# Performance work log

Measured on AMD Instinct MI355X. Metric: run time of the kernel, lower is better.

## Reference

```python
import jax, jax.numpy as jnp
import numpy as np

EPS = 1e-5


def _corr_matrix(A):
    # A: [n, f]. Standardize each column with unbiased std (torch.std default,
    # ddof=1), then all-pairs correlation as a single GEMM, matching
    # mean(x_std * y_std) over the batch dim for every column pair.
    n = A.shape[0]
    mu = A.mean(axis=0, keepdims=True)
    sd = A.std(axis=0, ddof=1, keepdims=True)
    As = (A - mu) / (sd + EPS)            # [n, f]
    return (As.T @ As) / n                 # [f, f]


def setup_inputs() -> dict:
    key = jax.random.key(0)
    kx, ky = jax.random.split(key)
    X = jax.random.normal(kx, (8192, 1024), dtype=jnp.float32)
    Y = jax.random.normal(ky, (8192, 1024), dtype=jnp.float32)
    return {"X": X, "Y": Y}


def reference(X, Y):
    f = X.shape[1]
    diff = _corr_matrix(X) - _corr_matrix(Y)          # [f, f]
    mask = jnp.triu(jnp.ones((f, f), dtype=diff.dtype), k=1)  # pairs i<j
    count = f * (f - 1) // 2
    loss = jnp.sum((diff * diff) * mask) / count
    return loss
```

## Files before the change

### kernel.cpp

```cpp
#include <hip/hip_runtime.h>
#include <hip/hip_bf16.h>
#include <stdint.h>

#define NROWS 8192
#define NF    1024
#define EPSV  1e-5f

typedef __attribute__((ext_vector_type(8))) short bf16x8;
typedef __attribute__((ext_vector_type(4))) float f32x4;

static __device__ __forceinline__ unsigned short f2bf(float v) {
    __hip_bfloat16 b = __float2bfloat16(v);
    return *reinterpret_cast<unsigned short*>(&b);
}

__global__ void stats_partial(const float* __restrict__ X, const float* __restrict__ Y,
                              float* __restrict__ psum, float* __restrict__ psq) {
    int cg    = blockIdx.x;
    int chunk = blockIdx.y;
    int mat   = blockIdx.z;
    const float* A = mat ? Y : X;
    int col = cg * 256 + threadIdx.x;
    const float* p = A + (size_t)(chunk * 128) * NF + col;
    float s = 0.f, sq = 0.f;
    #pragma unroll 4
    for (int i = 0; i < 128; ++i) {
        float v = p[(size_t)i * NF];
        s += v; sq += v * v;
    }
    int idx = (mat * 64 + chunk) * NF + col;
    psum[idx] = s;
    psq[idx]  = sq;
}

__global__ void stats_final(const float* __restrict__ psum, const float* __restrict__ psq,
                            float* __restrict__ mu, float* __restrict__ isd) {
    __shared__ float ls[4][64], lq[4][64];
    int mat  = blockIdx.y;
    int col0 = blockIdx.x * 64;
    int colq = threadIdx.x & 63;
    int g    = threadIdx.x >> 6;
    int col  = col0 + colq;
    float s = 0.f, sq = 0.f;
    #pragma unroll
    for (int k = 0; k < 16; ++k) {
        int idx = (mat * 64 + g * 16 + k) * NF + col;
        s  += psum[idx];
        sq += psq[idx];
    }
    ls[g][colq] = s; lq[g][colq] = sq;
    __syncthreads();
    if (g == 0) {
        s  = ls[0][colq] + ls[1][colq] + ls[2][colq] + ls[3][colq];
        sq = lq[0][colq] + lq[1][colq] + lq[2][colq] + lq[3][colq];
        float m   = s / (float)NROWS;
        float var = (sq - s * m) / (float)(NROWS - 1);
        var = fmaxf(var, 0.f);
        mu [mat * NF + col] = m;
        isd[mat * NF + col] = 1.0f / (sqrtf(var) + EPSV);
    }
}

__global__ void std_transpose(const float* __restrict__ X, const float* __restrict__ Y,
                              const float* __restrict__ mu, const float* __restrict__ isd,
                              unsigned short* __restrict__ Xst, unsigned short* __restrict__ Yst) {
    __shared__ unsigned short sbuf[64][68];
    __shared__ float smu[64], sisd[64];
    int ct  = blockIdx.x;
    int rt  = blockIdx.y;
    int mat = blockIdx.z;
    const float* A = mat ? Y : X;
    unsigned short* O = mat ? Yst : Xst;
    int tid = threadIdx.x;
    if (tid < 64) {
        smu[tid]  = mu [mat * NF + ct * 64 + tid];
        sisd[tid] = isd[mat * NF + ct * 64 + tid];
    }
    __syncthreads();
    #pragma unroll
    for (int it = 0; it < 4; ++it) {
        int idx = it * 256 + tid;
        int row = idx >> 4;
        int c4  = idx & 15;
        float4 v = *reinterpret_cast<const float4*>(
            A + (size_t)(rt * 64 + row) * NF + ct * 64 + c4 * 4);
        ushort4 o;
        o.x = f2bf((v.x - smu[c4 * 4 + 0]) * sisd[c4 * 4 + 0]);
        o.y = f2bf((v.y - smu[c4 * 4 + 1]) * sisd[c4 * 4 + 1]);
        o.z = f2bf((v.z - smu[c4 * 4 + 2]) * sisd[c4 * 4 + 2]);
        o.w = f2bf((v.w - smu[c4 * 4 + 3]) * sisd[c4 * 4 + 3]);
        *reinterpret_cast<ushort4*>(&sbuf[row][c4 * 4]) = o;
    }
    __syncthreads();
    {
        int c  = tid >> 2;
        int r8 = tid & 3;
        bf16x8 v0, v1;
        #pragma unroll
        for (int i = 0; i < 8; ++i) v0[i] = (short)sbuf[r8 * 16 + i][c];
        #pragma unroll
        for (int i = 0; i < 8; ++i) v1[i] = (short)sbuf[r8 * 16 + 8 + i][c];
        unsigned short* dst = O + (size_t)(ct * 64 + c) * NROWS + rt * 64 + r8 * 16;
        *reinterpret_cast<bf16x8*>(dst)     = v0;
        *reinterpret_cast<bf16x8*>(dst + 8) = v1;
    }
}

__global__ __launch_bounds__(256, 2) void gram_gemm(
    const unsigned short* __restrict__ Xst, const unsigned short* __restrict__ Yst,
    float* __restrict__ Cpart, int nsplit, int kper) {
    __shared__ short As[128 * 64];
    __shared__ short Bs[128 * 64];
    int tile = blockIdx.x, split = blockIdx.y, mat = blockIdx.z;
    int r = 0, t = tile;
    while (t >= 8 - r) { t -= 8 - r; ++r; }
    int c = r + t;
    const short* A = reinterpret_cast<const short*>(mat ? Yst : Xst);
    int tid = threadIdx.x, lane = tid & 63, wid = tid >> 6;
    int wr = wid >> 1, wc = wid & 1;
    f32x4 acc[4][4] = {};
    int k0 = split * kper;
    int nstep = kper >> 6;
    int r_loc = lane >> 3;
    int kc    = (lane & 7) ^ r_loc;

    for (int step = 0; step < nstep; ++step) {
        int kk = k0 + step * 64;
        __syncthreads();
        #pragma unroll
        for (int i = 0; i < 4; ++i) {
            int chunk = wid * 4 + i;
            int row = chunk * 8 + r_loc;
            const short* ga = A + (size_t)(r * 128 + row) * NROWS + kk + kc * 8;
            __builtin_amdgcn_global_load_lds(
                (const __attribute__((address_space(1))) void*)ga,
                (__attribute__((address_space(3))) void*)(As + chunk * 512), 16, 0, 0);
            const short* gb = A + (size_t)(c * 128 + row) * NROWS + kk + kc * 8;
            __builtin_amdgcn_global_load_lds(
                (const __attribute__((address_space(1))) void*)gb,
                (__attribute__((address_space(3))) void*)(Bs + chunk * 512), 16, 0, 0);
        }
        __syncthreads();
        bf16x8 af[4][2], bfr[4][2];
        #pragma unroll
        for (int fm = 0; fm < 4; ++fm) {
            int rowA = wr * 64 + fm * 16 + (lane & 15);
            int rowB = wc * 64 + fm * 16 + (lane & 15);
            #pragma unroll
            for (int h = 0; h < 2; ++h) {
                int kb = h * 4 + (lane >> 4);
                af [fm][h] = *reinterpret_cast<const bf16x8*>(
                    As + rowA * 64 + ((kb ^ (rowA & 7)) * 8));
                bfr[fm][h] = *reinterpret_cast<const bf16x8*>(
                    Bs + rowB * 64 + ((kb ^ (rowB & 7)) * 8));
            }
        }
        #pragma unroll
        for (int h = 0; h < 2; ++h)
            #pragma unroll
            for (int fm = 0; fm < 4; ++fm)
                #pragma unroll
                for (int fn = 0; fn < 4; ++fn)
                    acc[fm][fn] = __builtin_amdgcn_mfma_f32_16x16x32_bf16(
                        af[fm][h], bfr[fn][h], acc[fm][fn], 0, 0, 0);
    }

    float* Cp = Cpart + ((size_t)(mat * nsplit + split) * 36 + tile) * 16384;
    #pragma unroll
    for (int fm = 0; fm < 4; ++fm)
        #pragma unroll
        for (int fn = 0; fn < 4; ++fn)
            #pragma unroll
            for (int reg = 0; reg < 4; ++reg) {
                int row = wr * 64 + fm * 16 + (lane >> 4) * 4 + reg;
                int col = wc * 64 + fn * 16 + (lane & 15);
                Cp[row * 128 + col] = acc[fm][fn][reg];
            }
}

__global__ void reduce_loss(const float* __restrict__ Cpart, float* __restrict__ out,
                            int nsplit) {
    int tile = blockIdx.x, sub = blockIdx.y;
    int r = 0, t = tile;
    while (t >= 8 - r) { t -= 8 - r; ++r; }
    int c = r + t;
    const float inv_n = 1.0f / (float)NROWS;
    float s = 0.f;
    for (int e4 = threadIdx.x; e4 < 512; e4 += 256) {
        int row  = sub * 16 + (e4 >> 5);
        int col0 = (e4 & 31) * 4;
        float xs0 = 0.f, xs1 = 0.f, xs2 = 0.f, xs3 = 0.f;
        float ys0 = 0.f, ys1 = 0.f, ys2 = 0.f, ys3 = 0.f;
        for (int sp = 0; sp < nsplit; ++sp) {
            float4 vx = *reinterpret_cast<const float4*>(
                Cpart + ((size_t)sp * 36 + tile) * 16384 + row * 128 + col0);
            float4 vy = *reinterpret_cast<const float4*>(
                Cpart + ((size_t)(nsplit + sp) * 36 + tile) * 16384 + row * 128 + col0);
            xs0 += vx.x; xs1 += vx.y; xs2 += vx.z; xs3 += vx.w;
            ys0 += vy.x; ys1 += vy.y; ys2 += vy.z; ys3 += vy.w;
        }
        float dv[4] = {xs0 - ys0, xs1 - ys1, xs2 - ys2, xs3 - ys3};
        #pragma unroll
        for (int j = 0; j < 4; ++j) {
            int col = col0 + j;
            if (r == c && col <= row) continue;
            float d = dv[j] * inv_n;
            s += d * d;
        }
    }
    #pragma unroll
    for (int off = 32; off > 0; off >>= 1) s += __shfl_down(s, off, 64);
    __shared__ float wsum[4];
    int lane = threadIdx.x & 63, wid = threadIdx.x >> 6;
    if (lane == 0) wsum[wid] = s;
    __syncthreads();
    if (threadIdx.x == 0) {
        float tot = wsum[0] + wsum[1] + wsum[2] + wsum[3];
        atomicAdd(out, tot * (1.0f / 523776.0f));
    }
}

extern "C" void kernel_launch(void* const* d_in, const int* in_sizes, int n_in,
                              void* d_out, int out_size, void* d_ws, size_t ws_size,
                              hipStream_t stream) {
    const float* X = (const float*)d_in[0];
    const float* Y = (const float*)d_in[1];
    char* ws = (char*)d_ws;

    auto need = [](int ns) -> size_t {
        return ((size_t)32 << 20)
             + (size_t)2 * ns * 36 * 16384 * 4
             + ((size_t)512 << 10) * 2
             + ((size_t)8 << 10) * 2;
    };
    int nsplit = 8;
    if (ws_size < need(8)) nsplit = 4;
    if (ws_size < need(4)) nsplit = 2;
    if (ws_size < need(2)) nsplit = 1;
    int kper = NROWS / nsplit;

    unsigned short* Xst = (unsigned short*)(ws);
    unsigned short* Yst = (unsigned short*)(ws + ((size_t)16 << 20));
    float* Cpart = (float*)(ws + ((size_t)32 << 20));
    size_t cpart_sz = (size_t)2 * nsplit * 36 * 16384 * 4;
    float* psum = (float*)(ws + ((size_t)32 << 20) + cpart_sz);
    float* psq  = psum + 2 * 64 * NF;
    float* mu   = psq  + 2 * 64 * NF;
    float* isd  = mu   + 2 * NF;
    float* out  = (float*)d_out;

    hipMemsetAsync(out, 0, sizeof(float), stream);
    stats_partial<<<dim3(4, 64, 2), 256, 0, stream>>>(X, Y, psum, psq);
    stats_final<<<dim3(16, 2), 256, 0, stream>>>(psum, psq, mu, isd);
    std_transpose<<<dim3(16, 128, 2), 256, 0, stream>>>(X, Y, mu, isd, Xst, Yst);
    gram_gemm<<<dim3(36, nsplit, 2), 256, 0, stream>>>(Xst, Yst, Cpart, nsplit, kper);
    reduce_loss<<<dim3(36, 8), 256, 0, stream>>>(Cpart, out, nsplit);
}
```

Baseline: 179.2 us.

## Gram on raw bf16 data, apply standardization algebraically in fused double-buffered GEMM

Replaces the separate stats pass and standardize-transpose pass with one transpose kernel that converts raw inputs to bf16 and accumulates column sums from the bf16 values. The Gram GEMM now runs on unstandardized data and applies mean/std correction in its epilogue (C/n - mu_i mu_j) * isd_i * isd_j. X and Y are computed in the same workgroup with double-buffered LDS staging, and only their difference is written. This removes one full read pass over the inputs and halves partial-output traffic. In exchange, the centering is subtracted only after accumulation, so bf16 rounding of uncentered data can hurt accuracy when means are large. The split count also rises to 16 with an XCD-aware block swizzle.

```diff
diff --git a/kernel.cpp b/kernel.cpp
--- a/kernel.cpp
+++ b/kernel.cpp
@@ -13,24 +13,60 @@
     __hip_bfloat16 b = __float2bfloat16(v);
     return *reinterpret_cast<unsigned short*>(&b);
 }
-
-__global__ void stats_partial(const float* __restrict__ X, const float* __restrict__ Y,
-                              float* __restrict__ psum, float* __restrict__ psq) {
-    int cg    = blockIdx.x;
-    int chunk = blockIdx.y;
-    int mat   = blockIdx.z;
+static __device__ __forceinline__ float bf2f(unsigned short u) {
+    union { uint32_t i; float f; } cv; cv.i = (uint32_t)u << 16; return cv.f;
+}
+
+__global__ void transpose_stats(const float* __restrict__ X, const float* __restrict__ Y,
+                                unsigned short* __restrict__ Xst, unsigned short* __restrict__ Yst,
+                                float* __restrict__ psum, float* __restrict__ psq) {
+    __shared__ unsigned short sbuf[64][68];
+    int ct  = blockIdx.x;
+    int rt  = blockIdx.y;
+    int mat = blockIdx.z;
     const float* A = mat ? Y : X;
-    int col = cg * 256 + threadIdx.x;
-    const float* p = A + (size_t)(chunk * 128) * NF + col;
-    float s = 0.f, sq = 0.f;
-    #pragma unroll 4
-    for (int i = 0; i < 128; ++i) {
-        float v = p[(size_t)i * NF];
-        s += v; sq += v * v;
-    }
-    int idx = (mat * 64 + chunk) * NF + col;
-    psum[idx] = s;
-    psq[idx]  = sq;
+    unsigned short* O = mat ? Yst : Xst;
+    int tid = threadIdx.x;
+    #pragma unroll
+    for (int it = 0; it < 4; ++it) {
+        int idx = it * 256 + tid;
+        int row = idx >> 4;
+        int c4  = idx & 15;
+        float4 v = *reinterpret_cast<const float4*>(
+            A + (size_t)(rt * 64 + row) * NF + ct * 64 + c4 * 4);
+        ushort4 o;
+        o.x = f2bf(v.x); o.y = f2bf(v.y); o.z = f2bf(v.z); o.w = f2bf(v.w);
+        *reinterpret_cast<ushort4*>(&sbuf[row][c4 * 4]) = o;
+    }
+    __syncthreads();
+    {
+        int c  = tid >> 2;
+        int r8 = tid & 3;
+        bf16x8 v0, v1;
+        float s = 0.f, sq = 0.f;
+        #pragma unroll
+        for (int i = 0; i < 8; ++i) {
+            unsigned short u = sbuf[r8 * 16 + i][c];
+            v0[i] = (short)u;
+            float f = bf2f(u); s += f; sq += f * f;
+        }
+        #pragma unroll
+        for (int i = 0; i < 8; ++i) {
+            unsigned short u = sbuf[r8 * 16 + 8 + i][c];
+            v1[i] = (short)u;
+            float f = bf2f(u); s += f; sq += f * f;
+        }
+        unsigned short* dst = O + (size_t)(ct * 64 + c) * NROWS + rt * 64 + r8 * 16;
+        *reinterpret_cast<bf16x8*>(dst)     = v0;
+        *reinterpret_cast<bf16x8*>(dst + 8) = v1;
+        s  += __shfl_xor(s, 1);  s  += __shfl_xor(s, 2);
+        sq += __shfl_xor(sq, 1); sq += __shfl_xor(sq, 2);
+        if (r8 == 0) {
+            int pidx = (mat * 128 + rt) * NF + ct * 64 + c;
+            psum[pidx] = s;
+            psq[pidx]  = sq;
+        }
+    }
 }
 
 __global__ void stats_final(const float* __restrict__ psum, const float* __restrict__ psq,
@@ -43,8 +79,8 @@
     int col  = col0 + colq;
     float s = 0.f, sq = 0.f;
     #pragma unroll
-    for (int k = 0; k < 16; ++k) {
-        int idx = (mat * 64 + g * 16 + k) * NF + col;
+    for (int k = 0; k < 32; ++k) {
+        int idx = (mat * 128 + g * 32 + k) * NF + col;
         s  += psum[idx];
         sq += psq[idx];
     }
@@ -61,151 +97,131 @@
     }
 }
 
-__global__ void std_transpose(const float* __restrict__ X, const float* __restrict__ Y,
-                              const float* __restrict__ mu, const float* __restrict__ isd,
-                              unsigned short* __restrict__ Xst, unsigned short* __restrict__ Yst) {
-    __shared__ unsigned short sbuf[64][68];
-    __shared__ float smu[64], sisd[64];
-    int ct  = blockIdx.x;
-    int rt  = blockIdx.y;
-    int mat = blockIdx.z;
-    const float* A = mat ? Y : X;
-    unsigned short* O = mat ? Yst : Xst;
-    int tid = threadIdx.x;
-    if (tid < 64) {
-        smu[tid]  = mu [mat * NF + ct * 64 + tid];
-        sisd[tid] = isd[mat * NF + ct * 64 + tid];
-    }
-    __syncthreads();
-    #pragma unroll
-    for (int it = 0; it < 4; ++it) {
-        int idx = it * 256 + tid;
-        int row = idx >> 4;
-        int c4  = idx & 15;
-        float4 v = *reinterpret_cast<const float4*>(
-            A + (size_t)(rt * 64 + row) * NF + ct * 64 + c4 * 4);
-        ushort4 o;
-        o.x = f2bf((v.x - smu[c4 * 4 + 0]) * sisd[c4 * 4 + 0]);
-        o.y = f2bf((v.y - smu[c4 * 4 + 1]) * sisd[c4 * 4 + 1]);
-        o.z = f2bf((v.z - smu[c4 * 4 + 2]) * sisd[c4 * 4 + 2]);
-        o.w = f2bf((v.w - smu[c4 * 4 + 3]) * sisd[c4 * 4 + 3]);
-        *reinterpret_cast<ushort4*>(&sbuf[row][c4 * 4]) = o;
-    }
-    __syncthreads();
-    {
-        int c  = tid >> 2;
-        int r8 = tid & 3;
-        bf16x8 v0, v1;
-        #pragma unroll
-        for (int i = 0; i < 8; ++i) v0[i] = (short)sbuf[r8 * 16 + i][c];
-        #pragma unroll
-        for (int i = 0; i < 8; ++i) v1[i] = (short)sbuf[r8 * 16 + 8 + i][c];
-        unsigned short* dst = O + (size_t)(ct * 64 + c) * NROWS + rt * 64 + r8 * 16;
-        *reinterpret_cast<bf16x8*>(dst)     = v0;
-        *reinterpret_cast<bf16x8*>(dst + 8) = v1;
-    }
-}
-
-__global__ __launch_bounds__(256, 2) void gram_gemm(
+__global__ __launch_bounds__(256, 2) void gram_fused(
     const unsigned short* __restrict__ Xst, const unsigned short* __restrict__ Yst,
-    float* __restrict__ Cpart, int nsplit, int kper) {
-    __shared__ short As[128 * 64];
-    __shared__ short Bs[128 * 64];
-    int tile = blockIdx.x, split = blockIdx.y, mat = blockIdx.z;
-    int r = 0, t = tile;
-    while (t >= 8 - r) { t -= 8 - r; ++r; }
-    int c = r + t;
-    const short* A = reinterpret_cast<const short*>(mat ? Yst : Xst);
+    const float* __restrict__ mu, const float* __restrict__ isd,
+    float* __restrict__ Cdiff, int nsplit, int kper) {
+    __shared__ short lds[8][128 * 32];
+    int nwg = 36 * nsplit, cpx = nwg >> 3;
+    int bid = blockIdx.x;
+    int swz = (bid & 7) * cpx + (bid >> 3);
+    int split = swz / 36, tile = swz % 36;
+    int r = 0, t0 = tile;
+    while (t0 >= 8 - r) { t0 -= 8 - r; ++r; }
+    int c = r + t0;
+    const short* Xs = reinterpret_cast<const short*>(Xst);
+    const short* Ys = reinterpret_cast<const short*>(Yst);
     int tid = threadIdx.x, lane = tid & 63, wid = tid >> 6;
     int wr = wid >> 1, wc = wid & 1;
-    f32x4 acc[4][4] = {};
+    f32x4 accX[4][4] = {}, accY[4][4] = {};
     int k0 = split * kper;
-    int nstep = kper >> 6;
-    int r_loc = lane >> 3;
-    int kc    = (lane & 7) ^ r_loc;
-
-    for (int step = 0; step < nstep; ++step) {
-        int kk = k0 + step * 64;
-        __syncthreads();
-        #pragma unroll
-        for (int i = 0; i < 4; ++i) {
-            int chunk = wid * 4 + i;
-            int row = chunk * 8 + r_loc;
-            const short* ga = A + (size_t)(r * 128 + row) * NROWS + kk + kc * 8;
+    int nstep = kper >> 5;
+    int s8 = ((lane & 3) - (lane >> 3)) & 3;
+
+    auto stage = [&](const short* M, short* bA, short* bB, int ts) {
+        int kk = k0 + ts * 32;
+        #pragma unroll
+        for (int i = 0; i < 2; ++i) {
+            int chunk = wid * 2 + i;
+            int rw = chunk * 16 + (lane >> 2);
+            size_t ko = (size_t)kk + s8 * 8;
+            const short* ga = M + (size_t)(r * 128 + rw) * NROWS + ko;
             __builtin_amdgcn_global_load_lds(
                 (const __attribute__((address_space(1))) void*)ga,
-                (__attribute__((address_space(3))) void*)(As + chunk * 512), 16, 0, 0);
-            const short* gb = A + (size_t)(c * 128 + row) * NROWS + kk + kc * 8;
+                (__attribute__((address_space(3))) void*)(bA + chunk * 512), 16, 0, 0);
+            const short* gb = M + (size_t)(c * 128 + rw) * NROWS + ko;
             __builtin_amdgcn_global_load_lds(
                 (const __attribute__((address_space(1))) void*)gb,
-                (__attribute__((address_space(3))) void*)(Bs + chunk * 512), 16, 0, 0);
-        }
-        __syncthreads();
-        bf16x8 af[4][2], bfr[4][2];
-        #pragma unroll
-        for (int fm = 0; fm < 4; ++fm) {
-            int rowA = wr * 64 + fm * 16 + (lane & 15);
-            int rowB = wc * 64 + fm * 16 + (lane & 15);
+                (__attribute__((address_space(3))) void*)(bB + chunk * 512), 16, 0, 0);
+        }
+    };
+    auto compute = [&](const short* bA, const short* bB, f32x4 (&acc)[4][4]) {
+        bf16x8 a[4], b[4];
+        int rl = lane & 15;
+        int sl = ((lane >> 4) + (rl >> 1)) & 3;
+        #pragma unroll
+        for (int f = 0; f < 4; ++f) {
+            a[f] = *reinterpret_cast<const bf16x8*>(bA + (wr * 64 + f * 16 + rl) * 32 + sl * 8);
+            b[f] = *reinterpret_cast<const bf16x8*>(bB + (wc * 64 + f * 16 + rl) * 32 + sl * 8);
+        }
+        #pragma unroll
+        for (int fm = 0; fm < 4; ++fm)
             #pragma unroll
-            for (int h = 0; h < 2; ++h) {
-                int kb = h * 4 + (lane >> 4);
-                af [fm][h] = *reinterpret_cast<const bf16x8*>(
-                    As + rowA * 64 + ((kb ^ (rowA & 7)) * 8));
-                bfr[fm][h] = *reinterpret_cast<const bf16x8*>(
-                    Bs + rowB * 64 + ((kb ^ (rowB & 7)) * 8));
+            for (int fn = 0; fn < 4; ++fn)
+                acc[fm][fn] = __builtin_amdgcn_mfma_f32_16x16x32_bf16(
+                    a[fm], b[fn], acc[fm][fn], 0, 0, 0);
+    };
+
+    stage(Xs, lds[0], lds[2], 0);
+    stage(Ys, lds[4], lds[6], 0);
+    for (int t = 0; t < nstep; ++t) {
+        int cur = t & 1, nxt = cur ^ 1;
+        int tn = (t + 1) & (nstep - 1);
+        stage(Xs, lds[0 + nxt], lds[2 + nxt], tn);
+        asm volatile("s_waitcnt vmcnt(8)" ::: "memory");
+        __builtin_amdgcn_s_barrier();
+        __builtin_amdgcn_sched_barrier(0);
+        compute(lds[0 + cur], lds[2 + cur], accX);
+        stage(Ys, lds[4 + nxt], lds[6 + nxt], tn);
+        asm volatile("s_waitcnt vmcnt(8)" ::: "memory");
+        __builtin_amdgcn_s_barrier();
+        __builtin_amdgcn_sched_barrier(0);
+        compute(lds[4 + cur], lds[6 + cur], accY);
+    }
+    asm volatile("s_waitcnt vmcnt(0)" ::: "memory");
+
+    const float* mux = mu;        const float* muy = mu  + NF;
+    const float* isx = isd;       const float* isy = isd + NF;
+    const float inv_n = 1.0f / (float)NROWS;
+    float f0 = (split == 0) ? 1.0f : 0.0f;
+    float mxc[4], ixc[4], myc[4], iyc[4];
+    #pragma unroll
+    for (int fn = 0; fn < 4; ++fn) {
+        int cf = c * 128 + wc * 64 + fn * 16 + (lane & 15);
+        mxc[fn] = mux[cf]; ixc[fn] = isx[cf];
+        myc[fn] = muy[cf]; iyc[fn] = isy[cf];
+    }
+    float* Cp = Cdiff + ((size_t)split * 36 + tile) * 16384;
+    #pragma unroll
+    for (int fm = 0; fm < 4; ++fm)
+        #pragma unroll
+        for (int reg = 0; reg < 4; ++reg) {
+            int rf = r * 128 + wr * 64 + fm * 16 + (lane >> 4) * 4 + reg;
+            float mxr = mux[rf], ixr = isx[rf];
+            float myr = muy[rf], iyr = isy[rf];
+            int rowl = wr * 64 + fm * 16 + (lane >> 4) * 4 + reg;
+            #pragma unroll
+            for (int fn = 0; fn < 4; ++fn) {
+                float cx = (accX[fm][fn][reg] * inv_n - f0 * mxr * mxc[fn]) * ixr * ixc[fn];
+                float cy = (accY[fm][fn][reg] * inv_n - f0 * myr * myc[fn]) * iyr * iyc[fn];
+                int coll = wc * 64 + fn * 16 + (lane & 15);
+                Cp[rowl * 128 + coll] = cx - cy;
             }
         }
-        #pragma unroll
-        for (int h = 0; h < 2; ++h)
-            #pragma unroll
-            for (int fm = 0; fm < 4; ++fm)
-                #pragma unroll
-                for (int fn = 0; fn < 4; ++fn)
-                    acc[fm][fn] = __builtin_amdgcn_mfma_f32_16x16x32_bf16(
-                        af[fm][h], bfr[fn][h], acc[fm][fn], 0, 0, 0);
-    }
-
-    float* Cp = Cpart + ((size_t)(mat * nsplit + split) * 36 + tile) * 16384;
-    #pragma unroll
-    for (int fm = 0; fm < 4; ++fm)
-        #pragma unroll
-        for (int fn = 0; fn < 4; ++fn)
-            #pragma unroll
-            for (int reg = 0; reg < 4; ++reg) {
-                int row = wr * 64 + fm * 16 + (lane >> 4) * 4 + reg;
-                int col = wc * 64 + fn * 16 + (lane & 15);
-                Cp[row * 128 + col] = acc[fm][fn][reg];
-            }
-}
-
-__global__ void reduce_loss(const float* __restrict__ Cpart, float* __restrict__ out,
+}
+
+__global__ void reduce_loss(const float* __restrict__ Cdiff, float* __restrict__ out,
                             int nsplit) {
     int tile = blockIdx.x, sub = blockIdx.y;
     int r = 0, t = tile;
     while (t >= 8 - r) { t -= 8 - r; ++r; }
     int c = r + t;
-    const float inv_n = 1.0f / (float)NROWS;
     float s = 0.f;
     for (int e4 = threadIdx.x; e4 < 512; e4 += 256) {
         int row  = sub * 16 + (e4 >> 5);
         int col0 = (e4 & 31) * 4;
-        float xs0 = 0.f, xs1 = 0.f, xs2 = 0.f, xs3 = 0.f;
-        float ys0 = 0.f, ys1 = 0.f, ys2 = 0.f, ys3 = 0.f;
+        float d0 = 0.f, d1 = 0.f, d2 = 0.f, d3 = 0.f;
         for (int sp = 0; sp < nsplit; ++sp) {
-            float4 vx = *reinterpret_cast<const float4*>(
-                Cpart + ((size_t)sp * 36 + tile) * 16384 + row * 128 + col0);
-            float4 vy = *reinterpret_cast<const float4*>(
-                Cpart + ((size_t)(nsplit + sp) * 36 + tile) * 16384 + row * 128 + col0);
-            xs0 += vx.x; xs1 += vx.y; xs2 += vx.z; xs3 += vx.w;
-            ys0 += vy.x; ys1 += vy.y; ys2 += vy.z; ys3 += vy.w;
-        }
-        float dv[4] = {xs0 - ys0, xs1 - ys1, xs2 - ys2, xs3 - ys3};
+            float4 v = *reinterpret_cast<const float4*>(
+                Cdiff + ((size_t)sp * 36 + tile) * 16384 + row * 128 + col0);
+            d0 += v.x; d1 += v.y; d2 += v.z; d3 += v.w;
+        }
+        float dv[4] = {d0, d1, d2, d3};
         #pragma unroll
         for (int j = 0; j < 4; ++j) {
             int col = col0 + j;
             if (r == c && col <= row) continue;
-            float d = dv[j] * inv_n;
-            s += d * d;
+            s += dv[j] * dv[j];
         }
     }
     #pragma unroll
@@ -229,30 +245,28 @@
 
     auto need = [](int ns) -> size_t {
         return ((size_t)32 << 20)
-             + (size_t)2 * ns * 36 * 16384 * 4
-             + ((size_t)512 << 10) * 2
-             + ((size_t)8 << 10) * 2;
+             + (size_t)ns * 36 * 16384 * 4
+             + (size_t)2 * 128 * NF * 4 * 2
+             + (size_t)2 * NF * 4 * 2;
     };
-    int nsplit = 8;
-    if (ws_size < need(8)) nsplit = 4;
-    if (ws_size < need(4)) nsplit = 2;
-    if (ws_size < need(2)) nsplit = 1;
+    int nsplit = 16;
+    if (ws_size < need(16)) nsplit = 8;
+    if (ws_size < need(8))  nsplit = 4;
     int kper = NROWS / nsplit;
 
     unsigned short* Xst = (unsigned short*)(ws);
     unsigned short* Yst = (unsigned short*)(ws + ((size_t)16 << 20));
-    float* Cpart = (float*)(ws + ((size_t)32 << 20));
-    size_t cpart_sz = (size_t)2 * nsplit * 36 * 16384 * 4;
-    float* psum = (float*)(ws + ((size_t)32 << 20) + cpart_sz);
-    float* psq  = psum + 2 * 64 * NF;
-    float* mu   = psq  + 2 * 64 * NF;
+    float* Cdiff = (float*)(ws + ((size_t)32 << 20));
+    size_t cd_sz = (size_t)nsplit * 36 * 16384 * 4;
+    float* psum = (float*)(ws + ((size_t)32 << 20) + cd_sz);
+    float* psq  = psum + 2 * 128 * NF;
+    float* mu   = psq  + 2 * 128 * NF;
     float* isd  = mu   + 2 * NF;
     float* out  = (float*)d_out;
 
     hipMemsetAsync(out, 0, sizeof(float), stream);
-    stats_partial<<<dim3(4, 64, 2), 256, 0, stream>>>(X, Y, psum, psq);
+    transpose_stats<<<dim3(16, 128, 2), 256, 0, stream>>>(X, Y, Xst, Yst, psum, psq);
     stats_final<<<dim3(16, 2), 256, 0, stream>>>(psum, psq, mu, isd);
-    std_transpose<<<dim3(16, 128, 2), 256, 0, stream>>>(X, Y, mu, isd, Xst, Yst);
-    gram_gemm<<<dim3(36, nsplit, 2), 256, 0, stream>>>(Xst, Yst, Cpart, nsplit, kper);
-    reduce_loss<<<dim3(36, 8), 256, 0, stream>>>(Cpart, out, nsplit);
-}
+    gram_fused<<<36 * nsplit, 256, 0, stream>>>(Xst, Yst, mu, isd, Cdiff, nsplit, kper);
+    reduce_loss<<<dim3(36, 8), 256, 0, stream>>>(Cdiff, out, nsplit);
+}
```

Result: faster. 161.1 us (-10.1%).
